# Optimization experiments

Measured on AMD Instinct MI355X. Metric: run time of the kernel, lower is better.

## Reference

```python
import jax, jax.numpy as jnp
import numpy as np

N_ROIS = 1024
C, H, W = 512, 38, 50           # VGG16 conv5 feature map for a 608x800 image (stride 16)
IMG_H, IMG_W = 608.0, 800.0
POOLING_SIZE = 7                 # cfg.POOLING_SIZE


def setup_inputs() -> dict:
    key = jax.random.key(0)
    k1, k2 = jax.random.split(key, 2)
    bottom = jax.random.normal(k1, (1, C, H, W), dtype=jnp.float32)
    # Build valid ROI boxes (batch_idx, x1, y1, x2, y2) in image coordinates.
    u = jax.random.uniform(k2, (N_ROIS, 4), dtype=jnp.float32)
    x1 = u[:, 0] * (IMG_W - 32.0)
    y1 = u[:, 1] * (IMG_H - 32.0)
    x2 = x1 + 16.0 + u[:, 2] * (IMG_W - 16.0 - x1)
    y2 = y1 + 16.0 + u[:, 3] * (IMG_H - 16.0 - y1)
    rois = jnp.stack([jnp.zeros(N_ROIS, jnp.float32), x1, y1, x2, y2], axis=1)
    return {"bottom": bottom, "rois": rois, "pooling_size": POOLING_SIZE}


def _crop_pool(bottom, rois, pooling_size):
    """Faithful jax version of Network._crop_pool_layer (max_pool=True).
    affine_grid + grid_sample use align_corners=True semantics (old PyTorch
    default, which this theta parameterization assumes) with zeros padding.
    """
    Cc, Hh, Ww = bottom.shape[1], bottom.shape[2], bottom.shape[3]
    pre = pooling_size * 2
    x1 = rois[:, 1] / 16.0
    y1 = rois[:, 2] / 16.0
    x2 = rois[:, 3] / 16.0
    y2 = rois[:, 4] / 16.0
    # theta (separable: grid-x depends only on output col, grid-y only on row)
    t00 = (x2 - x1) / (Ww - 1)
    t02 = (x1 + x2 - Ww + 1) / (Ww - 1)
    t11 = (y2 - y1) / (Hh - 1)
    t12 = (y1 + y2 - Hh + 1) / (Hh - 1)
    base = jnp.linspace(-1.0, 1.0, pre)                 # align_corners=True base grid
    gx = t00[:, None] * base[None, :] + t02[:, None]     # [N, pre] normalized x
    gy = t11[:, None] * base[None, :] + t12[:, None]     # [N, pre] normalized y
    ix = (gx + 1.0) * 0.5 * (Ww - 1)                     # input pixel coords
    iy = (gy + 1.0) * 0.5 * (Hh - 1)
    x0 = jnp.floor(ix)
    y0 = jnp.floor(iy)
    ax = ix - x0
    ay = iy - y0
    x0i = x0.astype(jnp.int32); x1i = x0i + 1
    y0i = y0.astype(jnp.int32); y1i = y0i + 1

    def clip_w(idx, w, size):  # zeros-padding: out-of-bounds corners contribute 0
        valid = (idx >= 0) & (idx <= size - 1)
        return jnp.clip(idx, 0, size - 1), jnp.where(valid, w, 0.0)

    x0c, wx0 = clip_w(x0i, 1.0 - ax, Ww)
    x1c, wx1 = clip_w(x1i, ax, Ww)
    y0c, wy0 = clip_w(y0i, 1.0 - ay, Hh)
    y1c, wy1 = clip_w(y1i, ay, Hh)

    imgf = bottom[0].reshape(Cc, Hh * Ww)               # single image, expanded in torch

    def corner(yc, xc, wy, wx):
        idx = yc[:, :, None] * Ww + xc[:, None, :]      # [N, pre, pre]
        v = jnp.take(imgf, idx, axis=1)                 # [C, N, pre, pre]
        return v * (wy[:, :, None] * wx[:, None, :])[None]

    crops = (corner(y0c, x0c, wy0, wx0) + corner(y0c, x1c, wy0, wx1)
             + corner(y1c, x0c, wy1, wx0) + corner(y1c, x1c, wy1, wx1))
    crops = jnp.transpose(crops, (1, 0, 2, 3))          # [N, C, pre, pre]
    n = rois.shape[0]
    # F.max_pool2d(crops, 2, 2)
    pooled = crops.reshape(n, Cc, pooling_size, 2, pooling_size, 2).max(axis=(3, 5))
    return pooled


def reference(bottom, rois, pooling_size):
    return _crop_pool(bottom, rois, pooling_size)
```

## Files before the change

### kernel.cpp

```cpp
#include <hip/hip_runtime.h>
#include <hip/hip_fp16.h>
#include <float.h>

#define C_    512
#define H_    38
#define W_    50
#define HW_   (H_ * W_)
#define NROIS 1024
#define PS    7
#define PRE   14
#define NCELL 49
#define NGP   (PRE * PRE)
#define OTP   516

typedef float vfloat4 __attribute__((ext_vector_type(4)));
typedef _Float16 h2 __attribute__((ext_vector_type(2)));

__device__ inline h2 bch2u(unsigned v)   { return __builtin_bit_cast(h2, v); }
__device__ inline unsigned bcu(h2 v)     { return __builtin_bit_cast(unsigned, v); }

__global__ __launch_bounds__(256) void transpose_kernel(
    const float* __restrict__ in, _Float16* __restrict__ out) {
    __shared__ float tile[32][33];
    const int pix0 = blockIdx.x * 32;
    const int c0   = blockIdx.y * 32;
    const int tx = threadIdx.x & 31;
    const int ty = threadIdx.x >> 5;

    for (int i = ty; i < 32; i += 8) {
        int c = c0 + i, pix = pix0 + tx;
        tile[i][tx] = (pix < HW_) ? in[c * HW_ + pix] : 0.0f;
    }
    __syncthreads();
    for (int i = ty; i < 32; i += 8) {
        int pix = pix0 + i, c = c0 + tx;
        if (pix < HW_) out[pix * C_ + c] = (_Float16)tile[tx][i];
    }
}

__global__ __launch_bounds__(512, 4) void croppool_kernel(
    const _Float16* __restrict__ src, const float* __restrict__ rois,
    float* __restrict__ out) {

    const int n   = blockIdx.x;
    const int tid = threadIdx.x;

    __shared__ _Float16 outtile[NCELL * OTP];
    __shared__ int4  offt[NGP];
    __shared__ uint4 wgtt[NGP];

    if (tid < NGP) {
        const int gy = tid / PRE, gx = tid - PRE * gy;
        const float rx1 = rois[n * 5 + 1] * 0.0625f;
        const float ry1 = rois[n * 5 + 2] * 0.0625f;
        const float rx2 = rois[n * 5 + 3] * 0.0625f;
        const float ry2 = rois[n * 5 + 4] * 0.0625f;

        int xi0, xi1, yi0, yi1;
        float wx0, wx1, wy0, wy1;
        {
            const float sz = (float)(W_ - 1);
            const float t0 = (rx2 - rx1) / sz, tc = (rx1 + rx2 - sz) / sz;
            const float base = -1.0f + (float)gx * (2.0f / 13.0f);
            const float coord = (t0 * base + tc + 1.0f) * 0.5f * sz;
            const float f = floorf(coord), a = coord - f;
            const int i0 = (int)f, i1 = i0 + 1;
            wx0 = (i0 >= 0 && i0 <= W_ - 1) ? (1.0f - a) : 0.0f;
            wx1 = (i1 >= 0 && i1 <= W_ - 1) ? a : 0.0f;
            xi0 = min(max(i0, 0), W_ - 1);
            xi1 = min(max(i1, 0), W_ - 1);
        }
        {
            const float sz = (float)(H_ - 1);
            const float t0 = (ry2 - ry1) / sz, tc = (ry1 + ry2 - sz) / sz;
            const float base = -1.0f + (float)gy * (2.0f / 13.0f);
            const float coord = (t0 * base + tc + 1.0f) * 0.5f * sz;
            const float f = floorf(coord), a = coord - f;
            const int i0 = (int)f, i1 = i0 + 1;
            wy0 = (i0 >= 0 && i0 <= H_ - 1) ? (1.0f - a) : 0.0f;
            wy1 = (i1 >= 0 && i1 <= H_ - 1) ? a : 0.0f;
            yi0 = min(max(i0, 0), H_ - 1);
            yi1 = min(max(i1, 0), H_ - 1);
        }
        offt[tid] = make_int4((yi0 * W_ + xi0) * C_, (yi0 * W_ + xi1) * C_,
                              (yi1 * W_ + xi0) * C_, (yi1 * W_ + xi1) * C_);
        const _Float16 w0 = (_Float16)(wy0 * wx0);
        const _Float16 w1 = (_Float16)(wy0 * wx1);
        const _Float16 w2 = (_Float16)(wy1 * wx0);
        const _Float16 w3 = (_Float16)(wy1 * wx1);
        uint4 wv;
        wv.x = bcu((h2){w0, w0});
        wv.y = bcu((h2){w1, w1});
        wv.z = bcu((h2){w2, w2});
        wv.w = bcu((h2){w3, w3});
        wgtt[tid] = wv;
    }
    __syncthreads();

    const int lane = tid & 63;
    const int wave = tid >> 6;
    const _Float16* srcc = src + 8 * lane;

    for (int cell = wave; cell < NCELL; cell += 8) {
        const int py = cell / PS, px = cell - PS * py;
        const int gb = 2 * py * PRE + 2 * px;
        const int gps0 = gb, gps1 = gb + 1, gps2 = gb + PRE, gps3 = gb + PRE + 1;

        uint4 WV0 = wgtt[gps0], WV1 = wgtt[gps1], WV2 = wgtt[gps2], WV3 = wgtt[gps3];
        const int4 o0 = offt[gps0], o1 = offt[gps1], o2 = offt[gps2], o3 = offt[gps3];
        const uint4 V00 = *(const uint4*)(srcc + o0.x);
        const uint4 V01 = *(const uint4*)(srcc + o0.y);
        const uint4 V02 = *(const uint4*)(srcc + o0.z);
        const uint4 V03 = *(const uint4*)(srcc + o0.w);
        const uint4 V10 = *(const uint4*)(srcc + o1.x);
        const uint4 V11 = *(const uint4*)(srcc + o1.y);
        const uint4 V12 = *(const uint4*)(srcc + o1.z);
        const uint4 V13 = *(const uint4*)(srcc + o1.w);
        const uint4 V20 = *(const uint4*)(srcc + o2.x);
        const uint4 V21 = *(const uint4*)(srcc + o2.y);
        const uint4 V22 = *(const uint4*)(srcc + o2.z);
        const uint4 V23 = *(const uint4*)(srcc + o2.w);
        const uint4 V30 = *(const uint4*)(srcc + o3.x);
        const uint4 V31 = *(const uint4*)(srcc + o3.y);
        const uint4 V32 = *(const uint4*)(srcc + o3.z);
        const uint4 V33 = *(const uint4*)(srcc + o3.w);

        h2 m0, m1, m2, m3;
        {
            const h2 w0 = bch2u(WV0.x), w1 = bch2u(WV0.y), w2 = bch2u(WV0.z), w3 = bch2u(WV0.w);
            m0 = w0 * bch2u(V00.x) + w1 * bch2u(V01.x) + w2 * bch2u(V02.x) + w3 * bch2u(V03.x);
            m1 = w0 * bch2u(V00.y) + w1 * bch2u(V01.y) + w2 * bch2u(V02.y) + w3 * bch2u(V03.y);
            m2 = w0 * bch2u(V00.z) + w1 * bch2u(V01.z) + w2 * bch2u(V02.z) + w3 * bch2u(V03.z);
            m3 = w0 * bch2u(V00.w) + w1 * bch2u(V01.w) + w2 * bch2u(V02.w) + w3 * bch2u(V03.w);
        }
        {
            const h2 w0 = bch2u(WV1.x), w1 = bch2u(WV1.y), w2 = bch2u(WV1.z), w3 = bch2u(WV1.w);
            const h2 a0 = w0 * bch2u(V10.x) + w1 * bch2u(V11.x) + w2 * bch2u(V12.x) + w3 * bch2u(V13.x);
            const h2 a1 = w0 * bch2u(V10.y) + w1 * bch2u(V11.y) + w2 * bch2u(V12.y) + w3 * bch2u(V13.y);
            const h2 a2 = w0 * bch2u(V10.z) + w1 * bch2u(V11.z) + w2 * bch2u(V12.z) + w3 * bch2u(V13.z);
            const h2 a3 = w0 * bch2u(V10.w) + w1 * bch2u(V11.w) + w2 * bch2u(V12.w) + w3 * bch2u(V13.w);
            m0 = __builtin_elementwise_max(m0, a0);
            m1 = __builtin_elementwise_max(m1, a1);
            m2 = __builtin_elementwise_max(m2, a2);
            m3 = __builtin_elementwise_max(m3, a3);
        }
        {
            const h2 w0 = bch2u(WV2.x), w1 = bch2u(WV2.y), w2 = bch2u(WV2.z), w3 = bch2u(WV2.w);
            const h2 a0 = w0 * bch2u(V20.x) + w1 * bch2u(V21.x) + w2 * bch2u(V22.x) + w3 * bch2u(V23.x);
            const h2 a1 = w0 * bch2u(V20.y) + w1 * bch2u(V21.y) + w2 * bch2u(V22.y) + w3 * bch2u(V23.y);
            const h2 a2 = w0 * bch2u(V20.z) + w1 * bch2u(V21.z) + w2 * bch2u(V22.z) + w3 * bch2u(V23.z);
            const h2 a3 = w0 * bch2u(V20.w) + w1 * bch2u(V21.w) + w2 * bch2u(V22.w) + w3 * bch2u(V23.w);
            m0 = __builtin_elementwise_max(m0, a0);
            m1 = __builtin_elementwise_max(m1, a1);
            m2 = __builtin_elementwise_max(m2, a2);
            m3 = __builtin_elementwise_max(m3, a3);
        }
        {
            const h2 w0 = bch2u(WV3.x), w1 = bch2u(WV3.y), w2 = bch2u(WV3.z), w3 = bch2u(WV3.w);
            const h2 a0 = w0 * bch2u(V30.x) + w1 * bch2u(V31.x) + w2 * bch2u(V32.x) + w3 * bch2u(V33.x);
            const h2 a1 = w0 * bch2u(V30.y) + w1 * bch2u(V31.y) + w2 * bch2u(V32.y) + w3 * bch2u(V33.y);
            const h2 a2 = w0 * bch2u(V30.z) + w1 * bch2u(V31.z) + w2 * bch2u(V32.z) + w3 * bch2u(V33.z);
            const h2 a3 = w0 * bch2u(V30.w) + w1 * bch2u(V31.w) + w2 * bch2u(V32.w) + w3 * bch2u(V33.w);
            m0 = __builtin_elementwise_max(m0, a0);
            m1 = __builtin_elementwise_max(m1, a1);
            m2 = __builtin_elementwise_max(m2, a2);
            m3 = __builtin_elementwise_max(m3, a3);
        }

        _Float16* dst = &outtile[cell * OTP + 8 * lane];
        uint2 lo, hi;
        lo.x = bcu(m0); lo.y = bcu(m1);
        hi.x = bcu(m2); hi.y = bcu(m3);
        *(uint2*)dst       = lo;
        *(uint2*)(dst + 4) = hi;
    }
    __syncthreads();

    float* dstb = out + (size_t)n * (C_ * NCELL);
    for (int f = tid; f < C_ * NCELL; f += 512) {
        const int c = f / NCELL, cell = f - NCELL * c;
        __builtin_nontemporal_store((float)outtile[cell * OTP + c], &dstb[f]);
    }
}

__global__ __launch_bounds__(256) void croppool_fallback(
    const float* __restrict__ src, const float* __restrict__ rois,
    float* __restrict__ out) {

    const int n  = blockIdx.x >> 2;
    const int cq = blockIdx.x & 3;
    const int cbase = cq * 128;
    const int tid = threadIdx.x;

    __shared__ float outtile[128 * NCELL];
    __shared__ int   xi0[PRE], xi1[PRE], yi0[PRE], yi1[PRE];
    __shared__ float xw0[PRE], xw1[PRE], yw0[PRE], yw1[PRE];

    if (tid < 2 * PRE) {
        const int  j   = tid % PRE;
        const bool isy = tid >= PRE;
        const float r1 = rois[n * 5 + (isy ? 2 : 1)] * 0.0625f;
        const float r2 = rois[n * 5 + (isy ? 4 : 3)] * 0.0625f;
        const float sz = isy ? (float)(H_ - 1) : (float)(W_ - 1);
        const int  szi = isy ? (H_ - 1) : (W_ - 1);
        const float t0 = (r2 - r1) / sz;
        const float tc = (r1 + r2 - sz) / sz;
        const float base = -1.0f + (float)j * (2.0f / 13.0f);
        const float coord = (t0 * base + tc + 1.0f) * 0.5f * sz;
        const float f = floorf(coord);
        const float a = coord - f;
        const int i0 = (int)f;
        const int i1 = i0 + 1;
        const float w0 = (i0 >= 0 && i0 <= szi) ? (1.0f - a) : 0.0f;
        const float w1 = (i1 >= 0 && i1 <= szi) ? a : 0.0f;
        const int i0c = min(max(i0, 0), szi);
        const int i1c = min(max(i1, 0), szi);
        if (isy) { yi0[j] = i0c; yi1[j] = i1c; yw0[j] = w0; yw1[j] = w1; }
        else     { xi0[j] = i0c; xi1[j] = i1c; xw0[j] = w0; xw1[j] = w1; }
    }
    __syncthreads();

    const int wave = tid >> 6;
    const int lane = tid & 63;
    const float* srcc = src + (size_t)(cbase + lane) * HW_;

    for (int cell = wave; cell < NCELL; cell += 4) {
        const int py = cell / PS, px = cell % PS;
        float m0 = -FLT_MAX, m1 = -FLT_MAX;
        for (int ry = 0; ry < 2; ++ry) {
            const int gy = 2 * py + ry;
            for (int rx = 0; rx < 2; ++rx) {
                const int gx = 2 * px + rx;
                const int i00 = yi0[gy] * W_ + xi0[gx], i01 = yi0[gy] * W_ + xi1[gx];
                const int i10 = yi1[gy] * W_ + xi0[gx], i11 = yi1[gy] * W_ + xi1[gx];
                const float v0 = yw0[gy] * (xw0[gx] * srcc[i00] + xw1[gx] * srcc[i01])
                               + yw1[gy] * (xw0[gx] * srcc[i10] + xw1[gx] * srcc[i11]);
                const float v1 = yw0[gy] * (xw0[gx] * srcc[64 * HW_ + i00] + xw1[gx] * srcc[64 * HW_ + i01])
                               + yw1[gy] * (xw0[gx] * srcc[64 * HW_ + i10] + xw1[gx] * srcc[64 * HW_ + i11]);
                m0 = fmaxf(m0, v0);
                m1 = fmaxf(m1, v1);
            }
        }
        outtile[lane * NCELL + cell]        = m0;
        outtile[(lane + 64) * NCELL + cell] = m1;
    }
    __syncthreads();

    const vfloat4* lsrc = (const vfloat4*)outtile;
    vfloat4* dst = (vfloat4*)out + (size_t)n * (C_ * NCELL / 4) + cq * (128 * NCELL / 4);
    for (int i = tid; i < 128 * NCELL / 4; i += 256) {
        __builtin_nontemporal_store(lsrc[i], &dst[i]);
    }
}

extern "C" void kernel_launch(void* const* d_in, const int* in_sizes, int n_in,
                              void* d_out, int out_size, void* d_ws, size_t ws_size,
                              hipStream_t stream) {
    const float* bottom = (const float*)d_in[0];
    const float* rois   = (const float*)d_in[1];
    float* out = (float*)d_out;

    const size_t trans_bytes = (size_t)HW_ * C_ * sizeof(_Float16);
    if (ws_size >= trans_bytes) {
        _Float16* trans = (_Float16*)d_ws;
        dim3 tgrid((HW_ + 31) / 32, C_ / 32);
        transpose_kernel<<<tgrid, 256, 0, stream>>>(bottom, trans);
        croppool_kernel<<<NROIS, 512, 0, stream>>>(trans, rois, out);
    } else {
        croppool_fallback<<<NROIS * 4, 256, 0, stream>>>(bottom, rois, out);
    }
}
```

Before: 43.09 us.

## Split each ROI across two blocks and halve per-block register and LDS footprint

The crop-pool kernel now launches two blocks per ROI, each covering about half of the 49 pooled cells. Cell 24 is computed by both blocks and written with identical values. This halves the LDS output tile and raises the launch-bounds occupancy target. The sixteen bilinear gathers per cell are now issued as two batches of eight to lower register pressure. In exchange, each block recomputes the offset and weight tables, output stores become strided chunks of 25 floats per channel, and the cells split unevenly across waves.

```diff
diff --git a/kernel.cpp b/kernel.cpp
--- a/kernel.cpp
+++ b/kernel.cpp
@@ -12,6 +12,7 @@
 #define NCELL 49
 #define NGP   (PRE * PRE)
 #define OTP   516
+#define CPB   25
 
 typedef float vfloat4 __attribute__((ext_vector_type(4)));
 typedef _Float16 h2 __attribute__((ext_vector_type(2)));
@@ -38,14 +39,16 @@
     }
 }
 
-__global__ __launch_bounds__(512, 4) void croppool_kernel(
+__global__ __launch_bounds__(512, 8) void croppool_kernel(
     const _Float16* __restrict__ src, const float* __restrict__ rois,
     float* __restrict__ out) {
 
-    const int n   = blockIdx.x;
-    const int tid = threadIdx.x;
-
-    __shared__ _Float16 outtile[NCELL * OTP];
+    const int n    = blockIdx.x;
+    const int half = blockIdx.y;
+    const int cellLo = half * 24;
+    const int tid  = threadIdx.x;
+
+    __shared__ _Float16 outtile[CPB * OTP];
     __shared__ int4  offt[NGP];
     __shared__ uint4 wgtt[NGP];
 
@@ -101,73 +104,70 @@
     const int wave = tid >> 6;
     const _Float16* srcc = src + 8 * lane;
 
-    for (int cell = wave; cell < NCELL; cell += 8) {
+    for (int cl = wave; cl < CPB; cl += 8) {
+        const int cell = cellLo + cl;
         const int py = cell / PS, px = cell - PS * py;
         const int gb = 2 * py * PRE + 2 * px;
-        const int gps0 = gb, gps1 = gb + 1, gps2 = gb + PRE, gps3 = gb + PRE + 1;
-
-        uint4 WV0 = wgtt[gps0], WV1 = wgtt[gps1], WV2 = wgtt[gps2], WV3 = wgtt[gps3];
-        const int4 o0 = offt[gps0], o1 = offt[gps1], o2 = offt[gps2], o3 = offt[gps3];
-        const uint4 V00 = *(const uint4*)(srcc + o0.x);
-        const uint4 V01 = *(const uint4*)(srcc + o0.y);
-        const uint4 V02 = *(const uint4*)(srcc + o0.z);
-        const uint4 V03 = *(const uint4*)(srcc + o0.w);
-        const uint4 V10 = *(const uint4*)(srcc + o1.x);
-        const uint4 V11 = *(const uint4*)(srcc + o1.y);
-        const uint4 V12 = *(const uint4*)(srcc + o1.z);
-        const uint4 V13 = *(const uint4*)(srcc + o1.w);
-        const uint4 V20 = *(const uint4*)(srcc + o2.x);
-        const uint4 V21 = *(const uint4*)(srcc + o2.y);
-        const uint4 V22 = *(const uint4*)(srcc + o2.z);
-        const uint4 V23 = *(const uint4*)(srcc + o2.w);
-        const uint4 V30 = *(const uint4*)(srcc + o3.x);
-        const uint4 V31 = *(const uint4*)(srcc + o3.y);
-        const uint4 V32 = *(const uint4*)(srcc + o3.z);
-        const uint4 V33 = *(const uint4*)(srcc + o3.w);
 
         h2 m0, m1, m2, m3;
-        {
-            const h2 w0 = bch2u(WV0.x), w1 = bch2u(WV0.y), w2 = bch2u(WV0.z), w3 = bch2u(WV0.w);
-            m0 = w0 * bch2u(V00.x) + w1 * bch2u(V01.x) + w2 * bch2u(V02.x) + w3 * bch2u(V03.x);
-            m1 = w0 * bch2u(V00.y) + w1 * bch2u(V01.y) + w2 * bch2u(V02.y) + w3 * bch2u(V03.y);
-            m2 = w0 * bch2u(V00.z) + w1 * bch2u(V01.z) + w2 * bch2u(V02.z) + w3 * bch2u(V03.z);
-            m3 = w0 * bch2u(V00.w) + w1 * bch2u(V01.w) + w2 * bch2u(V02.w) + w3 * bch2u(V03.w);
-        }
-        {
-            const h2 w0 = bch2u(WV1.x), w1 = bch2u(WV1.y), w2 = bch2u(WV1.z), w3 = bch2u(WV1.w);
-            const h2 a0 = w0 * bch2u(V10.x) + w1 * bch2u(V11.x) + w2 * bch2u(V12.x) + w3 * bch2u(V13.x);
-            const h2 a1 = w0 * bch2u(V10.y) + w1 * bch2u(V11.y) + w2 * bch2u(V12.y) + w3 * bch2u(V13.y);
-            const h2 a2 = w0 * bch2u(V10.z) + w1 * bch2u(V11.z) + w2 * bch2u(V12.z) + w3 * bch2u(V13.z);
-            const h2 a3 = w0 * bch2u(V10.w) + w1 * bch2u(V11.w) + w2 * bch2u(V12.w) + w3 * bch2u(V13.w);
-            m0 = __builtin_elementwise_max(m0, a0);
-            m1 = __builtin_elementwise_max(m1, a1);
-            m2 = __builtin_elementwise_max(m2, a2);
-            m3 = __builtin_elementwise_max(m3, a3);
-        }
-        {
-            const h2 w0 = bch2u(WV2.x), w1 = bch2u(WV2.y), w2 = bch2u(WV2.z), w3 = bch2u(WV2.w);
-            const h2 a0 = w0 * bch2u(V20.x) + w1 * bch2u(V21.x) + w2 * bch2u(V22.x) + w3 * bch2u(V23.x);
-            const h2 a1 = w0 * bch2u(V20.y) + w1 * bch2u(V21.y) + w2 * bch2u(V22.y) + w3 * bch2u(V23.y);
-            const h2 a2 = w0 * bch2u(V20.z) + w1 * bch2u(V21.z) + w2 * bch2u(V22.z) + w3 * bch2u(V23.z);
-            const h2 a3 = w0 * bch2u(V20.w) + w1 * bch2u(V21.w) + w2 * bch2u(V22.w) + w3 * bch2u(V23.w);
-            m0 = __builtin_elementwise_max(m0, a0);
-            m1 = __builtin_elementwise_max(m1, a1);
-            m2 = __builtin_elementwise_max(m2, a2);
-            m3 = __builtin_elementwise_max(m3, a3);
-        }
-        {
-            const h2 w0 = bch2u(WV3.x), w1 = bch2u(WV3.y), w2 = bch2u(WV3.z), w3 = bch2u(WV3.w);
-            const h2 a0 = w0 * bch2u(V30.x) + w1 * bch2u(V31.x) + w2 * bch2u(V32.x) + w3 * bch2u(V33.x);
-            const h2 a1 = w0 * bch2u(V30.y) + w1 * bch2u(V31.y) + w2 * bch2u(V32.y) + w3 * bch2u(V33.y);
-            const h2 a2 = w0 * bch2u(V30.z) + w1 * bch2u(V31.z) + w2 * bch2u(V32.z) + w3 * bch2u(V33.z);
-            const h2 a3 = w0 * bch2u(V30.w) + w1 * bch2u(V31.w) + w2 * bch2u(V32.w) + w3 * bch2u(V33.w);
-            m0 = __builtin_elementwise_max(m0, a0);
-            m1 = __builtin_elementwise_max(m1, a1);
-            m2 = __builtin_elementwise_max(m2, a2);
-            m3 = __builtin_elementwise_max(m3, a3);
-        }
-
-        _Float16* dst = &outtile[cell * OTP + 8 * lane];
+
+        {
+            const int4  oa = offt[gb],  ob = offt[gb + 1];
+            const uint4 wa = wgtt[gb],  wb = wgtt[gb + 1];
+            const uint4 A0 = *(const uint4*)(srcc + oa.x);
+            const uint4 A1 = *(const uint4*)(srcc + oa.y);
+            const uint4 A2 = *(const uint4*)(srcc + oa.z);
+            const uint4 A3 = *(const uint4*)(srcc + oa.w);
+            const uint4 B0 = *(const uint4*)(srcc + ob.x);
+            const uint4 B1 = *(const uint4*)(srcc + ob.y);
+            const uint4 B2 = *(const uint4*)(srcc + ob.z);
+            const uint4 B3 = *(const uint4*)(srcc + ob.w);
+
+            {
+                const h2 w0 = bch2u(wa.x), w1 = bch2u(wa.y), w2 = bch2u(wa.z), w3 = bch2u(wa.w);
+                m0 = w0 * bch2u(A0.x) + w1 * bch2u(A1.x) + w2 * bch2u(A2.x) + w3 * bch2u(A3.x);
+                m1 = w0 * bch2u(A0.y) + w1 * bch2u(A1.y) + w2 * bch2u(A2.y) + w3 * bch2u(A3.y);
+                m2 = w0 * bch2u(A0.z) + w1 * bch2u(A1.z) + w2 * bch2u(A2.z) + w3 * bch2u(A3.z);
+                m3 = w0 * bch2u(A0.w) + w1 * bch2u(A1.w) + w2 * bch2u(A2.w) + w3 * bch2u(A3.w);
+            }
+            {
+                const h2 w0 = bch2u(wb.x), w1 = bch2u(wb.y), w2 = bch2u(wb.z), w3 = bch2u(wb.w);
+                m0 = __builtin_elementwise_max(m0, w0 * bch2u(B0.x) + w1 * bch2u(B1.x) + w2 * bch2u(B2.x) + w3 * bch2u(B3.x));
+                m1 = __builtin_elementwise_max(m1, w0 * bch2u(B0.y) + w1 * bch2u(B1.y) + w2 * bch2u(B2.y) + w3 * bch2u(B3.y));
+                m2 = __builtin_elementwise_max(m2, w0 * bch2u(B0.z) + w1 * bch2u(B1.z) + w2 * bch2u(B2.z) + w3 * bch2u(B3.z));
+                m3 = __builtin_elementwise_max(m3, w0 * bch2u(B0.w) + w1 * bch2u(B1.w) + w2 * bch2u(B2.w) + w3 * bch2u(B3.w));
+            }
+        }
+
+        {
+            const int4  oa = offt[gb + PRE],  ob = offt[gb + PRE + 1];
+            const uint4 wa = wgtt[gb + PRE],  wb = wgtt[gb + PRE + 1];
+            const uint4 A0 = *(const uint4*)(srcc + oa.x);
+            const uint4 A1 = *(const uint4*)(srcc + oa.y);
+            const uint4 A2 = *(const uint4*)(srcc + oa.z);
+            const uint4 A3 = *(const uint4*)(srcc + oa.w);
+            const uint4 B0 = *(const uint4*)(srcc + ob.x);
+            const uint4 B1 = *(const uint4*)(srcc + ob.y);
+            const uint4 B2 = *(const uint4*)(srcc + ob.z);
+            const uint4 B3 = *(const uint4*)(srcc + ob.w);
+
+            {
+                const h2 w0 = bch2u(wa.x), w1 = bch2u(wa.y), w2 = bch2u(wa.z), w3 = bch2u(wa.w);
+                m0 = __builtin_elementwise_max(m0, w0 * bch2u(A0.x) + w1 * bch2u(A1.x) + w2 * bch2u(A2.x) + w3 * bch2u(A3.x));
+                m1 = __builtin_elementwise_max(m1, w0 * bch2u(A0.y) + w1 * bch2u(A1.y) + w2 * bch2u(A2.y) + w3 * bch2u(A3.y));
+                m2 = __builtin_elementwise_max(m2, w0 * bch2u(A0.z) + w1 * bch2u(A1.z) + w2 * bch2u(A2.z) + w3 * bch2u(A3.z));
+                m3 = __builtin_elementwise_max(m3, w0 * bch2u(A0.w) + w1 * bch2u(A1.w) + w2 * bch2u(A2.w) + w3 * bch2u(A3.w));
+            }
+            {
+                const h2 w0 = bch2u(wb.x), w1 = bch2u(wb.y), w2 = bch2u(wb.z), w3 = bch2u(wb.w);
+                m0 = __builtin_elementwise_max(m0, w0 * bch2u(B0.x) + w1 * bch2u(B1.x) + w2 * bch2u(B2.x) + w3 * bch2u(B3.x));
+                m1 = __builtin_elementwise_max(m1, w0 * bch2u(B0.y) + w1 * bch2u(B1.y) + w2 * bch2u(B2.y) + w3 * bch2u(B3.y));
+                m2 = __builtin_elementwise_max(m2, w0 * bch2u(B0.z) + w1 * bch2u(B1.z) + w2 * bch2u(B2.z) + w3 * bch2u(B3.z));
+                m3 = __builtin_elementwise_max(m3, w0 * bch2u(B0.w) + w1 * bch2u(B1.w) + w2 * bch2u(B2.w) + w3 * bch2u(B3.w));
+            }
+        }
+
+        _Float16* dst = &outtile[cl * OTP + 8 * lane];
         uint2 lo, hi;
         lo.x = bcu(m0); lo.y = bcu(m1);
         hi.x = bcu(m2); hi.y = bcu(m3);
@@ -176,10 +176,10 @@
     }
     __syncthreads();
 
-    float* dstb = out + (size_t)n * (C_ * NCELL);
-    for (int f = tid; f < C_ * NCELL; f += 512) {
-        const int c = f / NCELL, cell = f - NCELL * c;
-        __builtin_nontemporal_store((float)outtile[cell * OTP + c], &dstb[f]);
+    float* dstb = out + (size_t)n * (C_ * NCELL) + cellLo;
+    for (int f = tid; f < C_ * CPB; f += 512) {
+        const int c = f / CPB, cl = f - CPB * c;
+        __builtin_nontemporal_store((float)outtile[cl * OTP + c], &dstb[c * NCELL + cl]);
     }
 }
 
@@ -265,7 +265,7 @@
         _Float16* trans = (_Float16*)d_ws;
         dim3 tgrid((HW_ + 31) / 32, C_ / 32);
         transpose_kernel<<<tgrid, 256, 0, stream>>>(bottom, trans);
-        croppool_kernel<<<NROIS, 512, 0, stream>>>(trans, rois, out);
+        croppool_kernel<<<dim3(NROIS, 2), 512, 0, stream>>>(trans, rois, out);
     } else {
         croppool_fallback<<<NROIS * 4, 256, 0, stream>>>(bottom, rois, out);
     }
```

Result: slower. 115.7 us (+168.5%).
